# Kernel optimization log

Hardware: AMD Instinct MI355X
Metric: run time of the kernel (lower is better)

## Reference

```python
import jax, jax.numpy as jnp
import numpy as np

SQRT_D = 8.0

def setup_inputs() -> dict:
    key = jax.random.key(0)
    kq, kk, kv = jax.random.split(key, 3)
    shape = (2, 16, 2048, 64)  # [batch, heads, seq, head_dim]
    return {
        "q": jax.random.normal(kq, shape, dtype=jnp.float32),
        "k": jax.random.normal(kk, shape, dtype=jnp.float32),
        "v": jax.random.normal(kv, shape, dtype=jnp.float32),
    }

def reference(q, k, v):
    # score = softmax(QK^T / sqrt_d) over the key axis j
    scores = jnp.einsum('bhif,bhjf->bhij', q, k) / SQRT_D
    probs = jax.nn.softmax(scores, axis=-1)
    # Note: original returns output permuted to [b, i, h, f]
    attn = jnp.einsum('bhij,bhjf->bihf', probs, v)
    return attn
```

## Files before the change

kernel.cpp:

```cpp
#include <hip/hip_runtime.h>

#define S_LEN 2048
#define HEADS 16
#define DIM 64

typedef __attribute__((ext_vector_type(8))) short short8;
typedef __attribute__((ext_vector_type(16))) float float16v;
typedef __attribute__((ext_vector_type(4))) float float4v;
typedef __attribute__((ext_vector_type(4))) unsigned uint4v;

static __device__ __forceinline__ unsigned pkbf(float lo, float hi) {
  unsigned r;
  asm("v_cvt_pk_bf16_f32 %0, %1, %2" : "=v"(r) : "v"(lo), "v"(hi));
  return r;
}

static __device__ __forceinline__ void gll16(const short* g, short* l) {
  __builtin_amdgcn_global_load_lds(
      (const __attribute__((address_space(1))) void*)g,
      (__attribute__((address_space(3))) void*)l, 16, 0, 0);
}

__global__ __launch_bounds__(256) void prep(const float* __restrict__ kk,
                                            const float* __restrict__ vv,
                                            short* __restrict__ kb,
                                            short* __restrict__ vt) {
  __shared__ unsigned t32[64 * 33];
  const int bx = blockIdx.x;
  const int bh = bx >> 5;
  const int j0 = (bx & 31) * 64;
  const int tid = threadIdx.x;

  {
    const int j = tid >> 2, f0 = (tid & 3) * 16;
    const float4v* src = (const float4v*)(kk + ((size_t)bh * S_LEN + j0 + j) * DIM + f0);
    float4v a0 = src[0], a1 = src[1], a2 = src[2], a3 = src[3];
    uint4v w0, w1;
    w0[0] = pkbf(a0[0], a0[1]); w0[1] = pkbf(a0[2], a0[3]);
    w0[2] = pkbf(a1[0], a1[1]); w0[3] = pkbf(a1[2], a1[3]);
    w1[0] = pkbf(a2[0], a2[1]); w1[1] = pkbf(a2[2], a2[3]);
    w1[2] = pkbf(a3[0], a3[1]); w1[3] = pkbf(a3[2], a3[3]);
    uint4v* dst = (uint4v*)(kb + ((size_t)bh * S_LEN + j0 + j) * DIM + f0);
    dst[0] = w0; dst[1] = w1;
  }
  {
    const int jp = (tid & 31) * 2, f0 = (tid >> 5) * 8;
    const int pp = ((jp & ~12) | ((jp & 4) << 1) | ((jp & 8) >> 1)) >> 1;
    const float* r0 = vv + ((size_t)bh * S_LEN + j0 + jp) * DIM + f0;
    const float* r1 = r0 + DIM;
    float4v a0 = *(const float4v*)r0, a1 = *(const float4v*)(r0 + 4);
    float4v b0 = *(const float4v*)r1, b1 = *(const float4v*)(r1 + 4);
#pragma unroll
    for (int e = 0; e < 4; e++) {
      t32[(f0 + e) * 33 + pp]     = pkbf(a0[e], b0[e]);
      t32[(f0 + 4 + e) * 33 + pp] = pkbf(a1[e], b1[e]);
    }
  }
  __syncthreads();
  {
    const int f = tid >> 2, x0 = (tid & 3) * 8;
    uint4v c0 = *(const uint4v*)&t32[f * 33 + x0];
    uint4v c1 = *(const uint4v*)&t32[f * 33 + x0 + 4];
    uint4v* dst = (uint4v*)(vt + ((size_t)bh * DIM + f) * S_LEN + j0 + x0 * 2);
    dst[0] = c0; dst[1] = c1;
  }
}

__global__ __launch_bounds__(128, 2) void attn_fwd(const float* __restrict__ q,
                                                   const short* __restrict__ kb,
                                                   const short* __restrict__ vt,
                                                   float* __restrict__ out) {
  __shared__ alignas(16) float smem[64 * 68];
  short* const k_lds = (short*)smem;
  short* const v_lds = k_lds + 4096;

  const int bx = blockIdx.x;
  const int bh = bx >> 5, it = bx & 31;
  const int b = bh >> 4, h = bh & 15;
  const int tid = threadIdx.x;
  const int w = tid >> 6, lane = tid & 63;
  const int n = lane & 31, hf = lane >> 5;
  const int i0 = it * 64 + w * 32;

  short8 qa[4];
  {
    const float* qrow = q + ((size_t)bh * S_LEN + i0 + n) * DIM + hf * 8;
#pragma unroll
    for (int ks = 0; ks < 4; ks++) {
      float4v x0 = *(const float4v*)(qrow + ks * 16);
      float4v x1 = *(const float4v*)(qrow + ks * 16 + 4);
      uint4v pk_;
      pk_[0] = pkbf(x0[0] * 0.125f, x0[1] * 0.125f);
      pk_[1] = pkbf(x0[2] * 0.125f, x0[3] * 0.125f);
      pk_[2] = pkbf(x1[0] * 0.125f, x1[1] * 0.125f);
      pk_[3] = pkbf(x1[2] * 0.125f, x1[3] * 0.125f);
      qa[ks] = *(short8*)&pk_;
    }
  }

  float16v acc0, acc1;
#pragma unroll
  for (int e = 0; e < 16; e++) { acc0[e] = 0.f; acc1[e] = 0.f; }
  float lp = 0.f;

  const short* kbase = kb + (size_t)bh * S_LEN * DIM;
  const short* vbase = vt + (size_t)bh * DIM * S_LEN;

  for (int j0 = 0; j0 < S_LEN; j0 += 64) {
    __syncthreads();
#pragma unroll
    for (int qi = 0; qi < 4; qi++) {
      const int ib = w * 4 + qi;
      const int jl = ib * 8 + (lane >> 3);
      const int ch = (lane & 7) ^ (jl & 7);
      gll16(kbase + (size_t)(j0 + jl) * DIM + ch * 8, &k_lds[ib * 512]);
      gll16(vbase + (size_t)jl * S_LEN + j0 + ch * 8, &v_lds[ib * 512]);
    }
    __syncthreads();

    float16v st0, st1;
#pragma unroll
    for (int e = 0; e < 16; e++) { st0[e] = 0.f; st1[e] = 0.f; }
#pragma unroll
    for (int ks = 0; ks < 4; ks++) {
      const int cpos = (2 * ks + hf) ^ (n & 7);
      short8 kf0 = *(const short8*)&k_lds[(n * 8 + cpos) * 8];
      short8 kf1 = *(const short8*)&k_lds[((32 + n) * 8 + cpos) * 8];
      st0 = __builtin_amdgcn_mfma_f32_32x32x16_bf16(kf0, qa[ks], st0, 0, 0, 0);
      st1 = __builtin_amdgcn_mfma_f32_32x32x16_bf16(kf1, qa[ks], st1, 0, 0, 0);
    }

#pragma unroll
    for (int e = 0; e < 16; e++) {
      st0[e] = __expf(st0[e]);
      st1[e] = __expf(st1[e]);
      lp += st0[e] + st1[e];
    }

    uint4v pb[4];
#pragma unroll
    for (int u = 0; u < 4; u++) {
      pb[0][u] = pkbf(st0[2 * u], st0[2 * u + 1]);
      pb[1][u] = pkbf(st0[8 + 2 * u], st0[8 + 2 * u + 1]);
      pb[2][u] = pkbf(st1[2 * u], st1[2 * u + 1]);
      pb[3][u] = pkbf(st1[8 + 2 * u], st1[8 + 2 * u + 1]);
    }

#pragma unroll
    for (int c = 0; c < 4; c++) {
      const int cpos = (2 * c + hf) ^ (n & 7);
      short8 vf0 = *(const short8*)&v_lds[(n * 8 + cpos) * 8];
      short8 vf1 = *(const short8*)&v_lds[((32 + n) * 8 + cpos) * 8];
      short8 pa = *(short8*)&pb[c];
      acc0 = __builtin_amdgcn_mfma_f32_32x32x16_bf16(vf0, pa, acc0, 0, 0, 0);
      acc1 = __builtin_amdgcn_mfma_f32_32x32x16_bf16(vf1, pa, acc1, 0, 0, 0);
    }
  }

  const float tot = lp + __shfl_xor(lp, 32);
  const float inv = 1.f / tot;

  __syncthreads();
  float* const ob = smem;
#pragma unroll
  for (int a = 0; a < 4; a++) {
    float4v t0, t1;
#pragma unroll
    for (int e = 0; e < 4; e++) {
      t0[e] = acc0[4 * a + e] * inv;
      t1[e] = acc1[4 * a + e] * inv;
    }
    const int row = w * 32 + n;
    *(float4v*)&ob[row * 68 + 8 * a + 4 * hf] = t0;
    *(float4v*)&ob[row * 68 + 32 + 8 * a + 4 * hf] = t1;
  }
  __syncthreads();
  {
    const int il = tid >> 1, fq = (tid & 1) * 32;
    const float* src = &ob[il * 68 + fq];
    float* dst = out + (((size_t)b * S_LEN + it * 64 + il) * HEADS + h) * DIM + fq;
#pragma unroll
    for (int u = 0; u < 8; u++) ((float4v*)dst)[u] = ((const float4v*)src)[u];
  }
}

extern "C" void kernel_launch(void* const* d_in, const int* in_sizes, int n_in,
                              void* d_out, int out_size, void* d_ws, size_t ws_size,
                              hipStream_t stream) {
  const float* q = (const float*)d_in[0];
  const float* k = (const float*)d_in[1];
  const float* v = (const float*)d_in[2];
  float* out = (float*)d_out;
  short* kb = (short*)d_ws;
  short* vt = (short*)d_ws + (size_t)32 * S_LEN * DIM;

  prep<<<1024, 256, 0, stream>>>(k, v, kb, vt);
  attn_fwd<<<1024, 128, 0, stream>>>(q, kb, vt, out);
}
```

Baseline: 145.8 us.

## Double-buffer K/V tiles in LDS, swizzle block order, use exp2 and MFMA row-sums

Splits LDS into two K/V buffers and issues global-to-LDS loads for the next tile before computing the current one, using explicit vmcnt waits and raw s_barrier calls so the loads overlap the MFMA work. It also remaps block indices so that consecutive blocks land on different head groups, and folds log2(e) into the Q scale so the exponential becomes a native exp2. The softmax denominator is now accumulated with an extra MFMA against a ones vector instead of a scalar sum and cross-lane shuffle. The cost is double the LDS footprint, which can lower occupancy, plus a third MFMA per V step, and the hand-written waitcnt counts are fragile if the compiler emits its own memory ops.

```diff
diff --git a/kernel.cpp b/kernel.cpp
--- a/kernel.cpp
+++ b/kernel.cpp
@@ -19,6 +19,12 @@
   __builtin_amdgcn_global_load_lds(
       (const __attribute__((address_space(1))) void*)g,
       (__attribute__((address_space(3))) void*)l, 16, 0, 0);
+}
+
+static __device__ __forceinline__ void bar() {
+  asm volatile("" ::: "memory");
+  __builtin_amdgcn_s_barrier();
+  asm volatile("" ::: "memory");
 }
 
 __global__ __launch_bounds__(256) void prep(const float* __restrict__ kk,
@@ -70,11 +76,13 @@
                                                    const short* __restrict__ kb,
                                                    const short* __restrict__ vt,
                                                    float* __restrict__ out) {
-  __shared__ alignas(16) float smem[64 * 68];
-  short* const k_lds = (short*)smem;
-  short* const v_lds = k_lds + 4096;
-
-  const int bx = blockIdx.x;
+  __shared__ alignas(16) float smem[8192];
+  short* const lds = (short*)smem;
+  short* const buf0 = lds;
+  short* const buf1 = lds + 8192;
+
+  const int bx0 = blockIdx.x;
+  const int bx = (bx0 & 7) * 128 + (bx0 >> 3);
   const int bh = bx >> 5, it = bx & 31;
   const int b = bh >> 4, h = bh & 15;
   const int tid = threadIdx.x;
@@ -84,59 +92,60 @@
 
   short8 qa[4];
   {
+    const float sc = 0.125f * 1.44269504088896f;
     const float* qrow = q + ((size_t)bh * S_LEN + i0 + n) * DIM + hf * 8;
 #pragma unroll
     for (int ks = 0; ks < 4; ks++) {
       float4v x0 = *(const float4v*)(qrow + ks * 16);
       float4v x1 = *(const float4v*)(qrow + ks * 16 + 4);
       uint4v pk_;
-      pk_[0] = pkbf(x0[0] * 0.125f, x0[1] * 0.125f);
-      pk_[1] = pkbf(x0[2] * 0.125f, x0[3] * 0.125f);
-      pk_[2] = pkbf(x1[0] * 0.125f, x1[1] * 0.125f);
-      pk_[3] = pkbf(x1[2] * 0.125f, x1[3] * 0.125f);
+      pk_[0] = pkbf(x0[0] * sc, x0[1] * sc);
+      pk_[1] = pkbf(x0[2] * sc, x0[3] * sc);
+      pk_[2] = pkbf(x1[0] * sc, x1[1] * sc);
+      pk_[3] = pkbf(x1[2] * sc, x1[3] * sc);
       qa[ks] = *(short8*)&pk_;
     }
   }
 
-  float16v acc0, acc1;
-#pragma unroll
-  for (int e = 0; e < 16; e++) { acc0[e] = 0.f; acc1[e] = 0.f; }
-  float lp = 0.f;
+  short8 ones;
+#pragma unroll
+  for (int e = 0; e < 8; e++) ones[e] = (short)0x3F80;
+
+  float16v acc0, acc1, accl;
+#pragma unroll
+  for (int e = 0; e < 16; e++) { acc0[e] = 0.f; acc1[e] = 0.f; accl[e] = 0.f; }
 
   const short* kbase = kb + (size_t)bh * S_LEN * DIM;
   const short* vbase = vt + (size_t)bh * DIM * S_LEN;
 
-  for (int j0 = 0; j0 < S_LEN; j0 += 64) {
-    __syncthreads();
+  auto stage = [&](short* dst, int j0) {
 #pragma unroll
     for (int qi = 0; qi < 4; qi++) {
       const int ib = w * 4 + qi;
       const int jl = ib * 8 + (lane >> 3);
       const int ch = (lane & 7) ^ (jl & 7);
-      gll16(kbase + (size_t)(j0 + jl) * DIM + ch * 8, &k_lds[ib * 512]);
-      gll16(vbase + (size_t)jl * S_LEN + j0 + ch * 8, &v_lds[ib * 512]);
-    }
-    __syncthreads();
-
+      gll16(kbase + (size_t)(j0 + jl) * DIM + ch * 8, dst + ib * 512);
+      gll16(vbase + (size_t)jl * S_LEN + j0 + ch * 8, dst + 4096 + ib * 512);
+    }
+  };
+
+  auto compute = [&](const short* kl, const short* vl) {
     float16v st0, st1;
 #pragma unroll
     for (int e = 0; e < 16; e++) { st0[e] = 0.f; st1[e] = 0.f; }
 #pragma unroll
     for (int ks = 0; ks < 4; ks++) {
       const int cpos = (2 * ks + hf) ^ (n & 7);
-      short8 kf0 = *(const short8*)&k_lds[(n * 8 + cpos) * 8];
-      short8 kf1 = *(const short8*)&k_lds[((32 + n) * 8 + cpos) * 8];
+      short8 kf0 = *(const short8*)&kl[(n * 8 + cpos) * 8];
+      short8 kf1 = *(const short8*)&kl[((32 + n) * 8 + cpos) * 8];
       st0 = __builtin_amdgcn_mfma_f32_32x32x16_bf16(kf0, qa[ks], st0, 0, 0, 0);
       st1 = __builtin_amdgcn_mfma_f32_32x32x16_bf16(kf1, qa[ks], st1, 0, 0, 0);
     }
-
 #pragma unroll
     for (int e = 0; e < 16; e++) {
-      st0[e] = __expf(st0[e]);
-      st1[e] = __expf(st1[e]);
-      lp += st0[e] + st1[e];
-    }
-
+      st0[e] = __builtin_amdgcn_exp2f(st0[e]);
+      st1[e] = __builtin_amdgcn_exp2f(st1[e]);
+    }
     uint4v pb[4];
 #pragma unroll
     for (int u = 0; u < 4; u++) {
@@ -145,20 +154,38 @@
       pb[2][u] = pkbf(st1[2 * u], st1[2 * u + 1]);
       pb[3][u] = pkbf(st1[8 + 2 * u], st1[8 + 2 * u + 1]);
     }
-
 #pragma unroll
     for (int c = 0; c < 4; c++) {
       const int cpos = (2 * c + hf) ^ (n & 7);
-      short8 vf0 = *(const short8*)&v_lds[(n * 8 + cpos) * 8];
-      short8 vf1 = *(const short8*)&v_lds[((32 + n) * 8 + cpos) * 8];
+      short8 vf0 = *(const short8*)&vl[(n * 8 + cpos) * 8];
+      short8 vf1 = *(const short8*)&vl[((32 + n) * 8 + cpos) * 8];
       short8 pa = *(short8*)&pb[c];
       acc0 = __builtin_amdgcn_mfma_f32_32x32x16_bf16(vf0, pa, acc0, 0, 0, 0);
       acc1 = __builtin_amdgcn_mfma_f32_32x32x16_bf16(vf1, pa, acc1, 0, 0, 0);
-    }
-  }
-
-  const float tot = lp + __shfl_xor(lp, 32);
-  const float inv = 1.f / tot;
+      accl = __builtin_amdgcn_mfma_f32_32x32x16_bf16(ones, pa, accl, 0, 0, 0);
+    }
+  };
+
+  stage(buf0, 0);
+#pragma unroll 1
+  for (int t = 0; t < 32; t += 2) {
+    stage(buf1, (t + 1) * 64);
+    asm volatile("s_waitcnt vmcnt(8)" ::: "memory");
+    bar();
+    compute(buf0, buf0 + 4096);
+    bar();
+    if (t + 2 < 32) {
+      stage(buf0, (t + 2) * 64);
+      asm volatile("s_waitcnt vmcnt(8)" ::: "memory");
+    } else {
+      asm volatile("s_waitcnt vmcnt(0)" ::: "memory");
+    }
+    bar();
+    compute(buf1, buf1 + 4096);
+    bar();
+  }
+
+  const float inv = 1.f / accl[0];
 
   __syncthreads();
   float* const ob = smem;
```

After: 139.1 us. -4.6%, faster.

## Split key range across waves with MFMA-fragment layout and register-direct loads

Applied to the files above, without the earlier changes.

The prep kernel now writes K and V^T in a layout matching the MFMA operand fragments, so the attention kernel can load fragments straight from global memory into registers without LDS staging or per-tile barriers. Each wave handles all 64 query rows but only half of the key sequence. The two waves' partial accumulators and row sums are combined through shared memory at the end. The change also folds log2(e) into the Q scale so exp2 can be used, prefetches the next K/V fragments during compute, raises MFMA priority with setprio, and remaps block indices for better L2 locality. The tradeoff is more registers per wave and global loads that the prefetch has to hide.

```diff
diff --git a/kernel.cpp b/kernel.cpp
--- a/kernel.cpp
+++ b/kernel.cpp
@@ -13,12 +13,6 @@
   unsigned r;
   asm("v_cvt_pk_bf16_f32 %0, %1, %2" : "=v"(r) : "v"(lo), "v"(hi));
   return r;
-}
-
-static __device__ __forceinline__ void gll16(const short* g, short* l) {
-  __builtin_amdgcn_global_load_lds(
-      (const __attribute__((address_space(1))) void*)g,
-      (__attribute__((address_space(3))) void*)l, 16, 0, 0);
 }
 
 __global__ __launch_bounds__(256) void prep(const float* __restrict__ kk,
@@ -40,8 +34,10 @@
     w0[2] = pkbf(a1[0], a1[1]); w0[3] = pkbf(a1[2], a1[3]);
     w1[0] = pkbf(a2[0], a2[1]); w1[1] = pkbf(a2[2], a2[3]);
     w1[2] = pkbf(a3[0], a3[1]); w1[3] = pkbf(a3[2], a3[3]);
-    uint4v* dst = (uint4v*)(kb + ((size_t)bh * S_LEN + j0 + j) * DIM + f0);
-    dst[0] = w0; dst[1] = w1;
+    short* dstb = kb + (size_t)bh * (S_LEN * DIM) +
+                  ((j0 >> 5) + (j >> 5)) * 2048 + (f0 >> 4) * 512 + (j & 31) * 8;
+    *(uint4v*)dstb = w0;
+    *(uint4v*)(dstb + 256) = w1;
   }
   {
     const int jp = (tid & 31) * 2, f0 = (tid >> 5) * 8;
@@ -61,8 +57,11 @@
     const int f = tid >> 2, x0 = (tid & 3) * 8;
     uint4v c0 = *(const uint4v*)&t32[f * 33 + x0];
     uint4v c1 = *(const uint4v*)&t32[f * 33 + x0 + 4];
-    uint4v* dst = (uint4v*)(vt + ((size_t)bh * DIM + f) * S_LEN + j0 + x0 * 2);
-    dst[0] = c0; dst[1] = c1;
+    const int jt = (j0 >> 5) + (x0 >> 4);
+    const int qd = (f >> 5) * 2 + ((x0 >> 3) & 1);
+    short* dstb = vt + (size_t)bh * (S_LEN * DIM) + jt * 2048 + qd * 512 + (f & 31) * 8;
+    *(uint4v*)dstb = c0;
+    *(uint4v*)(dstb + 256) = c1;
   }
 }
 
@@ -70,115 +69,153 @@
                                                    const short* __restrict__ kb,
                                                    const short* __restrict__ vt,
                                                    float* __restrict__ out) {
-  __shared__ alignas(16) float smem[64 * 68];
-  short* const k_lds = (short*)smem;
-  short* const v_lds = k_lds + 4096;
-
-  const int bx = blockIdx.x;
+  __shared__ alignas(16) float smem[8704];
+  const int bx0 = blockIdx.x;
+  const int bx = (bx0 & 7) * 128 + (bx0 >> 3);
   const int bh = bx >> 5, it = bx & 31;
   const int b = bh >> 4, h = bh & 15;
   const int tid = threadIdx.x;
   const int w = tid >> 6, lane = tid & 63;
   const int n = lane & 31, hf = lane >> 5;
-  const int i0 = it * 64 + w * 32;
-
-  short8 qa[4];
-  {
-    const float* qrow = q + ((size_t)bh * S_LEN + i0 + n) * DIM + hf * 8;
+  const int i0 = it * 64;
+
+  short8 qa0[4], qa1[4];
+  {
+    const float sc = 0.125f * 1.44269504088896f;
+    const float* qr = q + ((size_t)bh * S_LEN + i0 + n) * DIM + hf * 8;
 #pragma unroll
     for (int ks = 0; ks < 4; ks++) {
-      float4v x0 = *(const float4v*)(qrow + ks * 16);
-      float4v x1 = *(const float4v*)(qrow + ks * 16 + 4);
+      float4v x0 = *(const float4v*)(qr + ks * 16);
+      float4v x1 = *(const float4v*)(qr + ks * 16 + 4);
       uint4v pk_;
-      pk_[0] = pkbf(x0[0] * 0.125f, x0[1] * 0.125f);
-      pk_[1] = pkbf(x0[2] * 0.125f, x0[3] * 0.125f);
-      pk_[2] = pkbf(x1[0] * 0.125f, x1[1] * 0.125f);
-      pk_[3] = pkbf(x1[2] * 0.125f, x1[3] * 0.125f);
-      qa[ks] = *(short8*)&pk_;
-    }
-  }
-
-  float16v acc0, acc1;
-#pragma unroll
-  for (int e = 0; e < 16; e++) { acc0[e] = 0.f; acc1[e] = 0.f; }
-  float lp = 0.f;
-
-  const short* kbase = kb + (size_t)bh * S_LEN * DIM;
-  const short* vbase = vt + (size_t)bh * DIM * S_LEN;
-
-  for (int j0 = 0; j0 < S_LEN; j0 += 64) {
-    __syncthreads();
-#pragma unroll
-    for (int qi = 0; qi < 4; qi++) {
-      const int ib = w * 4 + qi;
-      const int jl = ib * 8 + (lane >> 3);
-      const int ch = (lane & 7) ^ (jl & 7);
-      gll16(kbase + (size_t)(j0 + jl) * DIM + ch * 8, &k_lds[ib * 512]);
-      gll16(vbase + (size_t)jl * S_LEN + j0 + ch * 8, &v_lds[ib * 512]);
-    }
-    __syncthreads();
-
-    float16v st0, st1;
-#pragma unroll
-    for (int e = 0; e < 16; e++) { st0[e] = 0.f; st1[e] = 0.f; }
-#pragma unroll
-    for (int ks = 0; ks < 4; ks++) {
-      const int cpos = (2 * ks + hf) ^ (n & 7);
-      short8 kf0 = *(const short8*)&k_lds[(n * 8 + cpos) * 8];
-      short8 kf1 = *(const short8*)&k_lds[((32 + n) * 8 + cpos) * 8];
-      st0 = __builtin_amdgcn_mfma_f32_32x32x16_bf16(kf0, qa[ks], st0, 0, 0, 0);
-      st1 = __builtin_amdgcn_mfma_f32_32x32x16_bf16(kf1, qa[ks], st1, 0, 0, 0);
-    }
+      pk_[0] = pkbf(x0[0] * sc, x0[1] * sc); pk_[1] = pkbf(x0[2] * sc, x0[3] * sc);
+      pk_[2] = pkbf(x1[0] * sc, x1[1] * sc); pk_[3] = pkbf(x1[2] * sc, x1[3] * sc);
+      qa0[ks] = *(short8*)&pk_;
+      float4v y0 = *(const float4v*)(qr + 32 * DIM + ks * 16);
+      float4v y1 = *(const float4v*)(qr + 32 * DIM + ks * 16 + 4);
+      pk_[0] = pkbf(y0[0] * sc, y0[1] * sc); pk_[1] = pkbf(y0[2] * sc, y0[3] * sc);
+      pk_[2] = pkbf(y1[0] * sc, y1[1] * sc); pk_[3] = pkbf(y1[2] * sc, y1[3] * sc);
+      qa1[ks] = *(short8*)&pk_;
+    }
+  }
+
+  const short* kp = kb + (size_t)bh * (S_LEN * DIM) + (size_t)w * (S_LEN * DIM / 2) + lane * 8;
+  const short* vp = vt + (size_t)bh * (S_LEN * DIM) + (size_t)w * (S_LEN * DIM / 2) + lane * 8;
+
+  short8 kf[4], vf[4];
+#pragma unroll
+  for (int u = 0; u < 4; u++) {
+    kf[u] = *(const short8*)(kp + u * 512);
+    vf[u] = *(const short8*)(vp + u * 512);
+  }
+
+  float16v zz;
+#pragma unroll
+  for (int e = 0; e < 16; e++) zz[e] = 0.f;
+  float16v a00 = zz, a01 = zz, a10 = zz, a11 = zz;
+  float lpa0 = 0.f, lpb0 = 0.f, lpa1 = 0.f, lpb1 = 0.f;
+
+#pragma unroll 1
+  for (int t = 0; t < 32; ++t) {
+    const int adv = (t < 31) ? 2048 : 0;
+    __builtin_amdgcn_s_setprio(1);
+    float16v st0 = __builtin_amdgcn_mfma_f32_32x32x16_bf16(kf[0], qa0[0], zz, 0, 0, 0);
+    float16v st1 = __builtin_amdgcn_mfma_f32_32x32x16_bf16(kf[0], qa1[0], zz, 0, 0, 0);
+#pragma unroll
+    for (int ks = 1; ks < 4; ks++) {
+      st0 = __builtin_amdgcn_mfma_f32_32x32x16_bf16(kf[ks], qa0[ks], st0, 0, 0, 0);
+      st1 = __builtin_amdgcn_mfma_f32_32x32x16_bf16(kf[ks], qa1[ks], st1, 0, 0, 0);
+    }
+    __builtin_amdgcn_s_setprio(0);
+    kp += adv;
+#pragma unroll
+    for (int u = 0; u < 4; u++) kf[u] = *(const short8*)(kp + u * 512);
 
 #pragma unroll
     for (int e = 0; e < 16; e++) {
-      st0[e] = __expf(st0[e]);
-      st1[e] = __expf(st1[e]);
-      lp += st0[e] + st1[e];
-    }
-
-    uint4v pb[4];
+      st0[e] = __builtin_amdgcn_exp2f(st0[e]);
+      st1[e] = __builtin_amdgcn_exp2f(st1[e]);
+    }
+#pragma unroll
+    for (int e = 0; e < 8; e++) {
+      lpa0 += st0[2 * e]; lpb0 += st0[2 * e + 1];
+      lpa1 += st1[2 * e]; lpb1 += st1[2 * e + 1];
+    }
+    uint4v pb00, pb01, pb10, pb11;
 #pragma unroll
     for (int u = 0; u < 4; u++) {
-      pb[0][u] = pkbf(st0[2 * u], st0[2 * u + 1]);
-      pb[1][u] = pkbf(st0[8 + 2 * u], st0[8 + 2 * u + 1]);
-      pb[2][u] = pkbf(st1[2 * u], st1[2 * u + 1]);
-      pb[3][u] = pkbf(st1[8 + 2 * u], st1[8 + 2 * u + 1]);
-    }
-
+      pb00[u] = pkbf(st0[2 * u], st0[2 * u + 1]);
+      pb01[u] = pkbf(st0[8 + 2 * u], st0[8 + 2 * u + 1]);
+      pb10[u] = pkbf(st1[2 * u], st1[2 * u + 1]);
+      pb11[u] = pkbf(st1[8 + 2 * u], st1[8 + 2 * u + 1]);
+    }
+    short8 p00 = *(short8*)&pb00, p01 = *(short8*)&pb01;
+    short8 p10 = *(short8*)&pb10, p11 = *(short8*)&pb11;
+
+    __builtin_amdgcn_s_setprio(1);
+    a00 = __builtin_amdgcn_mfma_f32_32x32x16_bf16(vf[0], p00, a00, 0, 0, 0);
+    a00 = __builtin_amdgcn_mfma_f32_32x32x16_bf16(vf[1], p01, a00, 0, 0, 0);
+    a01 = __builtin_amdgcn_mfma_f32_32x32x16_bf16(vf[0], p10, a01, 0, 0, 0);
+    a01 = __builtin_amdgcn_mfma_f32_32x32x16_bf16(vf[1], p11, a01, 0, 0, 0);
+    a10 = __builtin_amdgcn_mfma_f32_32x32x16_bf16(vf[2], p00, a10, 0, 0, 0);
+    a10 = __builtin_amdgcn_mfma_f32_32x32x16_bf16(vf[3], p01, a10, 0, 0, 0);
+    a11 = __builtin_amdgcn_mfma_f32_32x32x16_bf16(vf[2], p10, a11, 0, 0, 0);
+    a11 = __builtin_amdgcn_mfma_f32_32x32x16_bf16(vf[3], p11, a11, 0, 0, 0);
+    __builtin_amdgcn_s_setprio(0);
+    vp += adv;
+#pragma unroll
+    for (int u = 0; u < 4; u++) vf[u] = *(const short8*)(vp + u * 512);
+  }
+
+  float d0 = lpa0 + lpb0;
+  float d1 = lpa1 + lpb1;
+  d0 += __shfl_xor(d0, 32);
+  d1 += __shfl_xor(d1, 32);
+
+  float* const ob = smem;
+  float* const xb = smem + 4352;
+  float* const db = smem + 8448;
+
+  {
+    float16v sA = w ? a00 : a10;
+    float16v sB = w ? a01 : a11;
 #pragma unroll
     for (int c = 0; c < 4; c++) {
-      const int cpos = (2 * c + hf) ^ (n & 7);
-      short8 vf0 = *(const short8*)&v_lds[(n * 8 + cpos) * 8];
-      short8 vf1 = *(const short8*)&v_lds[((32 + n) * 8 + cpos) * 8];
-      short8 pa = *(short8*)&pb[c];
-      acc0 = __builtin_amdgcn_mfma_f32_32x32x16_bf16(vf0, pa, acc0, 0, 0, 0);
-      acc1 = __builtin_amdgcn_mfma_f32_32x32x16_bf16(vf1, pa, acc1, 0, 0, 0);
-    }
-  }
-
-  const float tot = lp + __shfl_xor(lp, 32);
-  const float inv = 1.f / tot;
-
+      float4v u0, u1;
+#pragma unroll
+      for (int e = 0; e < 4; e++) { u0[e] = sA[4 * c + e]; u1[e] = sB[4 * c + e]; }
+      *(float4v*)&xb[w * 2048 + c * 256 + lane * 4] = u0;
+      *(float4v*)&xb[w * 2048 + 1024 + c * 256 + lane * 4] = u1;
+    }
+    db[w * 128 + lane] = d0;
+    db[w * 128 + 64 + lane] = d1;
+  }
   __syncthreads();
-  float* const ob = smem;
-#pragma unroll
-  for (int a = 0; a < 4; a++) {
-    float4v t0, t1;
-#pragma unroll
-    for (int e = 0; e < 4; e++) {
-      t0[e] = acc0[4 * a + e] * inv;
-      t1[e] = acc1[4 * a + e] * inv;
-    }
-    const int row = w * 32 + n;
-    *(float4v*)&ob[row * 68 + 8 * a + 4 * hf] = t0;
-    *(float4v*)&ob[row * 68 + 32 + 8 * a + 4 * hf] = t1;
+  {
+    const int ow = 1 - w;
+    float16v mA = w ? a10 : a00;
+    float16v mB = w ? a11 : a01;
+    const float iv0 = 1.f / (d0 + db[ow * 128 + lane]);
+    const float iv1 = 1.f / (d1 + db[ow * 128 + 64 + lane]);
+#pragma unroll
+    for (int c = 0; c < 4; c++) {
+      float4v u0 = *(const float4v*)&xb[ow * 2048 + c * 256 + lane * 4];
+      float4v u1 = *(const float4v*)&xb[ow * 2048 + 1024 + c * 256 + lane * 4];
+      float4v t0, t1;
+#pragma unroll
+      for (int e = 0; e < 4; e++) {
+        t0[e] = (mA[4 * c + e] + u0[e]) * iv0;
+        t1[e] = (mB[4 * c + e] + u1[e]) * iv1;
+      }
+      *(float4v*)&ob[n * 68 + w * 32 + 8 * c + 4 * hf] = t0;
+      *(float4v*)&ob[(32 + n) * 68 + w * 32 + 8 * c + 4 * hf] = t1;
+    }
   }
   __syncthreads();
   {
     const int il = tid >> 1, fq = (tid & 1) * 32;
     const float* src = &ob[il * 68 + fq];
-    float* dst = out + (((size_t)b * S_LEN + it * 64 + il) * HEADS + h) * DIM + fq;
+    float* dst = out + (((size_t)b * S_LEN + i0 + il) * HEADS + h) * DIM + fq;
 #pragma unroll
     for (int u = 0; u < 8; u++) ((float4v*)dst)[u] = ((const float4v*)src)[u];
   }
```

Measured after the change: 134.6 us. 1.08x faster.
